# Kernel tuning notes

Hardware: AMD Instinct MI355X
Metric: run time of the kernel (lower is better)

The kernel has to match this reference:

```python
import jax, jax.numpy as jnp
import numpy as np

N_EMBD = 4096
N_HEAD = 2
HEAD_DIM = N_EMBD // N_HEAD  # 2048; note seq_len T must equal HEAD_DIM for the bias broadcast
B, T = 8, HEAD_DIM


def setup_inputs() -> dict:
    key = jax.random.key(0)
    ks = jax.random.split(key, 6)
    s = 1.0 / np.sqrt(N_EMBD)
    return {
        "x": jax.random.normal(ks[0], (B, T, N_EMBD), dtype=jnp.float32),
        "Wq": jax.random.normal(ks[1], (N_EMBD, N_EMBD), dtype=jnp.float32) * s,
        "Wk": jax.random.normal(ks[2], (N_EMBD, N_EMBD), dtype=jnp.float32) * s,
        "Wv": jax.random.normal(ks[3], (N_EMBD, N_EMBD), dtype=jnp.float32) * s,
        "Wo": jax.random.normal(ks[4], (N_EMBD, N_EMBD), dtype=jnp.float32) * s,
        "position_bias": jax.random.normal(ks[5], (N_HEAD, HEAD_DIM), dtype=jnp.float32) * 0.02,
    }


def reference(x, Wq, Wk, Wv, Wo, position_bias):
    Bb, Tt, C = x.shape
    H, D = N_HEAD, C // N_HEAD
    # nn.Linear(bias=False): y = x @ W.T
    q = (x @ Wq.T).reshape(Bb, Tt, H, D).transpose(0, 2, 1, 3)  # (B,H,T,D)
    k = (x @ Wk.T).reshape(Bb, Tt, H, D).transpose(0, 2, 1, 3)
    v = (x @ Wv.T).reshape(Bb, Tt, H, D).transpose(0, 2, 1, 3)
    scale = 1.0 / jnp.sqrt(jnp.asarray(D, dtype=x.dtype))
    scores = jnp.einsum("bhtd,bhsd->bhts", q, k) * scale  # (B,H,T,T)
    # position_bias (H,D) -> (1,H,1,D); broadcasts over key axis since D == T
    scores = scores + position_bias[None, :, None, :]
    atten = jax.nn.softmax(scores, axis=-1)  # mask=None, dropout=0.0 -> identity
    y = jnp.einsum("bhts,bhsd->bhtd", atten, v)  # (B,H,T,D)
    y = y.transpose(0, 2, 1, 3).reshape(Bb, Tt, C)
    y = y @ Wo.T
    return (y, atten)
```

## Files before the change

kernel.cpp:

```cpp
#include <hip/hip_runtime.h>
#include <hip/hip_bf16.h>
#include <cstdint>
#include <cstddef>


typedef short short8_t __attribute__((ext_vector_type(8)));
typedef float f32x4   __attribute__((ext_vector_type(4)));

__device__ __forceinline__ short f2bf(float f) {
  unsigned u = __builtin_bit_cast(unsigned, f);
  u = (u + 0x7FFFu + ((u >> 16) & 1u)) >> 16;
  return (short)u;
}

__device__ __forceinline__ short8_t cvt8(f32x4 a, f32x4 b) {
  short8_t r;
  r[0] = f2bf(a[0]); r[1] = f2bf(a[1]); r[2] = f2bf(a[2]); r[3] = f2bf(a[3]);
  r[4] = f2bf(b[0]); r[5] = f2bf(b[1]); r[6] = f2bf(b[2]); r[7] = f2bf(b[3]);
  return r;
}

__device__ __forceinline__ void gld_lds16(const void* g, void* l) {
  __builtin_amdgcn_global_load_lds(
      (const __attribute__((address_space(1))) void*)g,
      (__attribute__((address_space(3))) void*)l, 16, 0, 0);
}

__global__ __launch_bounds__(256)
void cvt_f32_bf16(const float* __restrict__ src, short* __restrict__ dst, int n8) {
  for (int i = blockIdx.x * blockDim.x + threadIdx.x; i < n8;
       i += gridDim.x * blockDim.x) {
    const f32x4* p = (const f32x4*)(src + (size_t)i * 8);
    f32x4 a = __builtin_nontemporal_load(p);
    f32x4 b = __builtin_nontemporal_load(p + 1);
    *(short8_t*)(dst + (size_t)i * 8) = cvt8(a, b);
  }
}

template<int MODE>
__global__ __launch_bounds__(512, 2)
void gemm256(const short* __restrict__ Ag, const short* __restrict__ Bg,
             void* __restrict__ Cg, const float* __restrict__ bias) {
  constexpr int K  = (MODE == 3 || MODE == 4) ? 2048 : 4096;
  constexpr int NS = K / 32;

  __shared__ short lds[65536];

  const int tid = threadIdx.x;

  const int bid = blockIdx.x;
  const int id  = (bid & 7) * (gridDim.x >> 3) + (bid >> 3);

  int m0, n0, z = 0;
  size_t aoff = 0, boff = 0;
  if constexpr (MODE == 3 || MODE == 4) {
    z  = id >> 6;
    m0 = ((id >> 3) & 7) << 8;
    n0 = (id & 7) << 8;
    aoff = boff = (size_t)z << 22;
  } else {
    m0 = (id >> 4) << 8;
    n0 = (id & 15) << 8;
  }

  const int r0 = tid >> 2;
  const int qs = ((tid & 3) ^ ((r0 >> 1) & 3)) << 3;
  const short* Ap0 = Ag + aoff + (size_t)(m0 + r0) * K + qs;
  const short* Ap1 = Ap0 + (size_t)128 * K;
  const short* Bp0 = Bg + boff + (size_t)(n0 + r0) * K + qs;
  const short* Bp1 = Bp0 + (size_t)128 * K;
  short* la0 = &lds[0]    + tid * 8;
  short* la1 = la0 + 4096;
  short* lb0 = &lds[8192] + tid * 8;
  short* lb1 = lb0 + 4096;

  auto STAGE = [&](int t) {
    const int s = (t & 3) * 16384;
    const int k = t * 32;
    gld_lds16(Ap0 + k, la0 + s);
    gld_lds16(Ap1 + k, la1 + s);
    gld_lds16(Bp0 + k, lb0 + s);
    gld_lds16(Bp1 + k, lb1 + s);
  };

  const int l  = tid & 63;
  const int fr = l & 15;
  const int kq = l >> 4;
  const int wm = (tid >> 8) << 7;
  const int wn = ((tid >> 6) & 3) << 6;
  const int slotP = (kq ^ ((fr >> 1) & 3)) << 3;
  const int aB = (wm + fr) * 32 + slotP;
  const int bB = 8192 + (wn + fr) * 32 + slotP;

  f32x4 acc[8][4] = {};
  short8_t fA[8], fB[4], gA[8], gB[4];

  auto phase = [&](int p, short8_t (&cA)[8], short8_t (&cB)[4],
                   short8_t (&nA)[8], short8_t (&nB)[4]) {
    if (p + 2 < NS) {
      asm volatile("s_waitcnt vmcnt(4)" ::: "memory");
    } else {
      asm volatile("s_waitcnt vmcnt(0)" ::: "memory");
    }
    __builtin_amdgcn_s_barrier();
    if (p + 3 < NS) STAGE(p + 3);
    if (p + 1 < NS) {
      const short* sl = &lds[((p + 1) & 3) * 16384];
#pragma unroll
      for (int m = 0; m < 8; ++m) nA[m] = *(const short8_t*)&sl[aB + m * 512];
#pragma unroll
      for (int n = 0; n < 4; ++n) nB[n] = *(const short8_t*)&sl[bB + n * 512];
    }
    __builtin_amdgcn_s_setprio(1);
#pragma unroll
    for (int m = 0; m < 8; ++m)
#pragma unroll
      for (int n = 0; n < 4; ++n)
        acc[m][n] = __builtin_amdgcn_mfma_f32_16x16x32_bf16(cA[m], cB[n], acc[m][n], 0, 0, 0);
    __builtin_amdgcn_s_setprio(0);
  };

  STAGE(0); STAGE(1); STAGE(2);
  asm volatile("s_waitcnt vmcnt(8)" ::: "memory");
  __builtin_amdgcn_s_barrier();
  {
    const short* sl = &lds[0];
#pragma unroll
    for (int m = 0; m < 8; ++m) fA[m] = *(const short8_t*)&sl[aB + m * 512];
#pragma unroll
    for (int n = 0; n < 4; ++n) fB[n] = *(const short8_t*)&sl[bB + n * 512];
  }

  for (int p = 0; p < NS; p += 2) {
    phase(p,     fA, fB, gA, gB);
    phase(p + 1, gA, gB, fA, fB);
  }

#pragma unroll
  for (int m = 0; m < 8; ++m) {
#pragma unroll
    for (int n = 0; n < 4; ++n) {
#pragma unroll
      for (int r = 0; r < 4; ++r) {
        const int gm = m0 + wm + m * 16 + kq * 4 + r;
        const int gn = n0 + wn + n * 16 + fr;
        const float v = acc[m][n][r];
        if constexpr (MODE == 0) {
          short* dst = (short*)Cg;
          const int bh = ((gm >> 11) << 1) + (gn >> 11);
          __builtin_nontemporal_store(f2bf(v),
            &dst[((size_t)bh << 22) + ((size_t)(gm & 2047) << 11) + (gn & 2047)]);
        } else if constexpr (MODE == 2) {
          short* dst = (short*)Cg;
          const int bh = ((gm >> 11) << 1) + (gn >> 11);
          __builtin_nontemporal_store(f2bf(v),
            &dst[((size_t)bh << 22) + ((size_t)(gn & 2047) << 11) + (gm & 2047)]);
        } else if constexpr (MODE == 3) {
          float* dst = (float*)Cg;
          const float sv = v * 0.022097086912079608f + bias[((z & 1) << 11) + gn];
          __builtin_nontemporal_store(sv,
            &dst[((size_t)z << 22) + ((size_t)gm << 11) + gn]);
        } else if constexpr (MODE == 4) {
          short* dst = (short*)Cg;
          const size_t row = ((size_t)(z >> 1) << 11) + gm;
          __builtin_nontemporal_store(f2bf(v),
            &dst[(row << 12) + ((size_t)(z & 1) << 11) + gn]);
        } else {
          float* dst = (float*)Cg;
          __builtin_nontemporal_store(v, &dst[(size_t)gm * 4096 + gn]);
        }
      }
    }
  }
}

__global__ __launch_bounds__(256)
void softmax_rows(float* __restrict__ attn, short* __restrict__ outb) {
  float* row  = attn + ((size_t)blockIdx.x << 11);
  short* rowb = outb + ((size_t)blockIdx.x << 11);
  const int tid = threadIdx.x;

  f32x4 v0 = __builtin_nontemporal_load((const f32x4*)(row + tid * 8));
  f32x4 v1 = __builtin_nontemporal_load((const f32x4*)(row + tid * 8 + 4));

  float m = fmaxf(fmaxf(fmaxf(v0[0], v0[1]), fmaxf(v0[2], v0[3])),
                  fmaxf(fmaxf(v1[0], v1[1]), fmaxf(v1[2], v1[3])));
#pragma unroll
  for (int off = 1; off < 64; off <<= 1) m = fmaxf(m, __shfl_xor(m, off));

  __shared__ float redm[4];
  __shared__ float reds[4];
  if ((tid & 63) == 0) redm[tid >> 6] = m;
  __syncthreads();
  m = fmaxf(fmaxf(redm[0], redm[1]), fmaxf(redm[2], redm[3]));

  float e[8];
#pragma unroll
  for (int i = 0; i < 4; ++i) e[i]     = expf(v0[i] - m);
#pragma unroll
  for (int i = 0; i < 4; ++i) e[4 + i] = expf(v1[i] - m);
  float s = 0.f;
#pragma unroll
  for (int i = 0; i < 8; ++i) s += e[i];
#pragma unroll
  for (int off = 1; off < 64; off <<= 1) s += __shfl_xor(s, off);
  if ((tid & 63) == 0) reds[tid >> 6] = s;
  __syncthreads();
  s = reds[0] + reds[1] + reds[2] + reds[3];

  const float inv = 1.0f / s;
  f32x4 o0, o1;
#pragma unroll
  for (int i = 0; i < 4; ++i) { o0[i] = e[i] * inv; o1[i] = e[4 + i] * inv; }
  __builtin_nontemporal_store(o0, (f32x4*)(row + tid * 8));
  __builtin_nontemporal_store(o1, (f32x4*)(row + tid * 8 + 4));
  *(short8_t*)(rowb + tid * 8) = cvt8(o0, o1);
}

extern "C" void kernel_launch(void* const* d_in, const int* in_sizes, int n_in,
                              void* d_out, int out_size, void* d_ws, size_t ws_size,
                              hipStream_t stream) {
  const float* x  = (const float*)d_in[0];
  const float* Wq = (const float*)d_in[1];
  const float* Wk = (const float*)d_in[2];
  const float* Wv = (const float*)d_in[3];
  const float* Wo = (const float*)d_in[4];
  const float* pb = (const float*)d_in[5];

  float* y_out = (float*)d_out;
  float* attn  = y_out + (size_t)8 * 2048 * 4096;

  const size_t NEED = 4ull * 67108864ull * 2ull;
  if (ws_size < NEED) return;
  short* buf0 = (short*)d_ws;
  short* buf1 = buf0 + 67108864;
  short* buf2 = buf1 + 67108864;
  short* buf3 = buf2 + 67108864;

  short* xb      = buf0;
  short* qb      = buf1;
  short* kb      = buf2;
  short* vtb     = buf3;
  short* wob     = buf0;
  short* attn_bf = buf1;
  short* yb      = buf2;
  short* wb      = (short*)attn;

  const dim3 blk512(512);
  const dim3 blk(256);
  const dim3 gcv(2048);
  const dim3 g1k(1024);

  cvt_f32_bf16<<<gcv, blk, 0, stream>>>(x, xb, 67108864 / 8);

  cvt_f32_bf16<<<gcv, blk, 0, stream>>>(Wq, wb, 16777216 / 8);
  gemm256<0><<<g1k, blk512, 0, stream>>>(xb, wb, qb, nullptr);
  cvt_f32_bf16<<<gcv, blk, 0, stream>>>(Wk, wb, 16777216 / 8);
  gemm256<0><<<g1k, blk512, 0, stream>>>(xb, wb, kb, nullptr);
  cvt_f32_bf16<<<gcv, blk, 0, stream>>>(Wv, wb, 16777216 / 8);
  gemm256<2><<<g1k, blk512, 0, stream>>>(xb, wb, vtb, nullptr);

  cvt_f32_bf16<<<gcv, blk, 0, stream>>>(Wo, wob, 16777216 / 8);

  gemm256<3><<<g1k, blk512, 0, stream>>>(qb, kb, attn, pb);
  softmax_rows<<<dim3(32768), blk, 0, stream>>>(attn, attn_bf);
  gemm256<4><<<g1k, blk512, 0, stream>>>(attn_bf, vtb, yb, nullptr);
  gemm256<5><<<g1k, blk512, 0, stream>>>(yb, wob, y_out, nullptr);
}
```

Before: 2.922 ms.

## Rework GEMM to 256 threads with 128x128 warp tiles and new LDS layout

Switches the 256x256-tile GEMM from 512 threads (8 waves, 128x64 per wave) to 256 threads (4 waves, 128x128 per wave, 64 accumulators per lane). It replaces the XOR-swizzled row-major LDS layout with a fragment-ordered layout where each lane reads a contiguous 16-byte chunk. It also drops the register double-buffered fragment prefetch in favour of a simpler single-stage load-then-MFMA loop. The goal is higher MFMA-to-LDS-read ratio per wave, at the cost of very high register pressure, one block per CU, and less latency hiding between LDS reads and MFMAs.

After: 3.347 ms. 1.15x slower.

```diff
diff --git a/kernel.cpp b/kernel.cpp
--- a/kernel.cpp
+++ b/kernel.cpp
@@ -38,7 +38,7 @@
 }
 
 template<int MODE>
-__global__ __launch_bounds__(512, 2)
+__global__ __launch_bounds__(256, 1)
 void gemm256(const short* __restrict__ Ag, const short* __restrict__ Bg,
              void* __restrict__ Cg, const float* __restrict__ bias) {
   constexpr int K  = (MODE == 3 || MODE == 4) ? 2048 : 4096;
@@ -63,83 +63,68 @@
     n0 = (id & 15) << 8;
   }
 
-  const int r0 = tid >> 2;
-  const int qs = ((tid & 3) ^ ((r0 >> 1) & 3)) << 3;
-  const short* Ap0 = Ag + aoff + (size_t)(m0 + r0) * K + qs;
-  const short* Ap1 = Ap0 + (size_t)128 * K;
-  const short* Bp0 = Bg + boff + (size_t)(n0 + r0) * K + qs;
-  const short* Bp1 = Bp0 + (size_t)128 * K;
-  short* la0 = &lds[0]    + tid * 8;
-  short* la1 = la0 + 4096;
-  short* lb0 = &lds[8192] + tid * 8;
-  short* lb1 = lb0 + 4096;
+  const int l = tid & 63;
+  const int w = tid >> 6;
+
+  const int srow = l & 15;
+  const int skol = (l >> 4) * 8;
+  const short* ApS = Ag + aoff + (size_t)(m0 + 64 * w + srow) * K + skol;
+  const short* BpS = Bg + boff + (size_t)(n0 + 64 * w + srow) * K + skol;
+  short* laS = &lds[(4 * w) * 512 + l * 8];
+  short* lbS = &lds[8192 + (4 * w) * 512 + l * 8];
 
   auto STAGE = [&](int t) {
-    const int s = (t & 3) * 16384;
-    const int k = t * 32;
-    gld_lds16(Ap0 + k, la0 + s);
-    gld_lds16(Ap1 + k, la1 + s);
-    gld_lds16(Bp0 + k, lb0 + s);
-    gld_lds16(Bp1 + k, lb1 + s);
+    const int s = (t & 3) << 14;
+    const size_t k = (size_t)t * 32;
+#pragma unroll
+    for (int j = 0; j < 4; ++j) {
+      gld_lds16(ApS + (size_t)j * 16 * K + k, laS + j * 512 + s);
+      gld_lds16(BpS + (size_t)j * 16 * K + k, lbS + j * 512 + s);
+    }
   };
 
-  const int l  = tid & 63;
+  const int aU = (w >> 1) * 8;
+  const int bU = (w & 1) * 8;
+  const int l8 = l * 8;
+
+  f32x4 acc[8][8] = {};
+
+  STAGE(0); STAGE(1); STAGE(2);
+
+  for (int p = 0; p < NS; ++p) {
+    if (p + 2 < NS)      asm volatile("s_waitcnt vmcnt(16)" ::: "memory");
+    else if (p + 1 < NS) asm volatile("s_waitcnt vmcnt(8)" ::: "memory");
+    else                 asm volatile("s_waitcnt vmcnt(0)" ::: "memory");
+    __builtin_amdgcn_s_barrier();
+
+    if (p + 3 < NS) STAGE(p + 3);
+
+    const int slot = (p & 3) << 14;
+    short8_t A[8], B[8];
+#pragma unroll
+    for (int i = 0; i < 8; ++i)
+      A[i] = *(const short8_t*)&lds[slot + (aU + i) * 512 + l8];
+#pragma unroll
+    for (int j = 0; j < 8; ++j)
+      B[j] = *(const short8_t*)&lds[slot + 8192 + (bU + j) * 512 + l8];
+
+    __builtin_amdgcn_s_setprio(1);
+#pragma unroll
+    for (int m = 0; m < 8; ++m)
+#pragma unroll
+      for (int n = 0; n < 8; ++n)
+        acc[m][n] = __builtin_amdgcn_mfma_f32_16x16x32_bf16(A[m], B[n], acc[m][n], 0, 0, 0);
+    __builtin_amdgcn_s_setprio(0);
+  }
+
   const int fr = l & 15;
   const int kq = l >> 4;
-  const int wm = (tid >> 8) << 7;
-  const int wn = ((tid >> 6) & 3) << 6;
-  const int slotP = (kq ^ ((fr >> 1) & 3)) << 3;
-  const int aB = (wm + fr) * 32 + slotP;
-  const int bB = 8192 + (wn + fr) * 32 + slotP;
-
-  f32x4 acc[8][4] = {};
-  short8_t fA[8], fB[4], gA[8], gB[4];
-
-  auto phase = [&](int p, short8_t (&cA)[8], short8_t (&cB)[4],
-                   short8_t (&nA)[8], short8_t (&nB)[4]) {
-    if (p + 2 < NS) {
-      asm volatile("s_waitcnt vmcnt(4)" ::: "memory");
-    } else {
-      asm volatile("s_waitcnt vmcnt(0)" ::: "memory");
-    }
-    __builtin_amdgcn_s_barrier();
-    if (p + 3 < NS) STAGE(p + 3);
-    if (p + 1 < NS) {
-      const short* sl = &lds[((p + 1) & 3) * 16384];
-#pragma unroll
-      for (int m = 0; m < 8; ++m) nA[m] = *(const short8_t*)&sl[aB + m * 512];
-#pragma unroll
-      for (int n = 0; n < 4; ++n) nB[n] = *(const short8_t*)&sl[bB + n * 512];
-    }
-    __builtin_amdgcn_s_setprio(1);
-#pragma unroll
-    for (int m = 0; m < 8; ++m)
-#pragma unroll
-      for (int n = 0; n < 4; ++n)
-        acc[m][n] = __builtin_amdgcn_mfma_f32_16x16x32_bf16(cA[m], cB[n], acc[m][n], 0, 0, 0);
-    __builtin_amdgcn_s_setprio(0);
-  };
-
-  STAGE(0); STAGE(1); STAGE(2);
-  asm volatile("s_waitcnt vmcnt(8)" ::: "memory");
-  __builtin_amdgcn_s_barrier();
-  {
-    const short* sl = &lds[0];
-#pragma unroll
-    for (int m = 0; m < 8; ++m) fA[m] = *(const short8_t*)&sl[aB + m * 512];
-#pragma unroll
-    for (int n = 0; n < 4; ++n) fB[n] = *(const short8_t*)&sl[bB + n * 512];
-  }
-
-  for (int p = 0; p < NS; p += 2) {
-    phase(p,     fA, fB, gA, gB);
-    phase(p + 1, gA, gB, fA, fB);
-  }
-
+  const int wm = (w >> 1) << 7;
+  const int wn = (w & 1) << 7;
 #pragma unroll
   for (int m = 0; m < 8; ++m) {
 #pragma unroll
-    for (int n = 0; n < 4; ++n) {
+    for (int n = 0; n < 8; ++n) {
 #pragma unroll
       for (int r = 0; r < 4; ++r) {
         const int gm = m0 + wm + m * 16 + kq * 4 + r;
@@ -246,7 +231,6 @@
   short* yb      = buf2;
   short* wb      = (short*)attn;
 
-  const dim3 blk512(512);
   const dim3 blk(256);
   const dim3 gcv(2048);
   const dim3 g1k(1024);
@@ -254,16 +238,16 @@
   cvt_f32_bf16<<<gcv, blk, 0, stream>>>(x, xb, 67108864 / 8);
 
   cvt_f32_bf16<<<gcv, blk, 0, stream>>>(Wq, wb, 16777216 / 8);
-  gemm256<0><<<g1k, blk512, 0, stream>>>(xb, wb, qb, nullptr);
+  gemm256<0><<<g1k, blk, 0, stream>>>(xb, wb, qb, nullptr);
   cvt_f32_bf16<<<gcv, blk, 0, stream>>>(Wk, wb, 16777216 / 8);
-  gemm256<0><<<g1k, blk512, 0, stream>>>(xb, wb, kb, nullptr);
+  gemm256<0><<<g1k, blk, 0, stream>>>(xb, wb, kb, nullptr);
   cvt_f32_bf16<<<gcv, blk, 0, stream>>>(Wv, wb, 16777216 / 8);
-  gemm256<2><<<g1k, blk512, 0, stream>>>(xb, wb, vtb, nullptr);
+  gemm256<2><<<g1k, blk, 0, stream>>>(xb, wb, vtb, nullptr);
 
   cvt_f32_bf16<<<gcv, blk, 0, stream>>>(Wo, wob, 16777216 / 8);
 
-  gemm256<3><<<g1k, blk512, 0, stream>>>(qb, kb, attn, pb);
+  gemm256<3><<<g1k, blk, 0, stream>>>(qb, kb, attn, pb);
   softmax_rows<<<dim3(32768), blk, 0, stream>>>(attn, attn_bf);
-  gemm256<4><<<g1k, blk512, 0, stream>>>(attn_bf, vtb, yb, nullptr);
-  gemm256<5><<<g1k, blk512, 0, stream>>>(yb, wob, y_out, nullptr);
-}
+  gemm256<4><<<g1k, blk, 0, stream>>>(attn_bf, vtb, yb, nullptr);
+  gemm256<5><<<g1k, blk, 0, stream>>>(yb, wob, y_out, nullptr);
+}
```

## Switch GEMM to 32x32x16 MFMA with fragment-native LDS layout

Applied to the files above, without the earlier changes.

Replaces the 16x16x32 bf16 MFMA tiling with 32x32x16 MFMAs, using 4x2 accumulator tiles of 16 floats per wave. The global-to-LDS staging is rearranged so each wave writes 32-row by 16-k fragments contiguously, and each lane reads its operand fragment with a linear 16-byte LDS load. This drops the XOR swizzle. The aim is fewer MFMA issues and fewer LDS reads per unit of work. The risk is LDS bank conflicts from the unswizzled layout and a more scattered epilogue store pattern.

After: 3.576 ms. +22.4%, slower.

```diff
diff --git a/kernel.cpp b/kernel.cpp
--- a/kernel.cpp
+++ b/kernel.cpp
@@ -6,6 +6,7 @@
 
 typedef short short8_t __attribute__((ext_vector_type(8)));
 typedef float f32x4   __attribute__((ext_vector_type(4)));
+typedef float f32x16  __attribute__((ext_vector_type(16)));
 
 __device__ __forceinline__ short f2bf(float f) {
   unsigned u = __builtin_bit_cast(unsigned, f);
@@ -63,88 +64,88 @@
     n0 = (id & 15) << 8;
   }
 
-  const int r0 = tid >> 2;
-  const int qs = ((tid & 3) ^ ((r0 >> 1) & 3)) << 3;
-  const short* Ap0 = Ag + aoff + (size_t)(m0 + r0) * K + qs;
-  const short* Ap1 = Ap0 + (size_t)128 * K;
-  const short* Bp0 = Bg + boff + (size_t)(n0 + r0) * K + qs;
-  const short* Bp1 = Bp0 + (size_t)128 * K;
-  short* la0 = &lds[0]    + tid * 8;
-  short* la1 = la0 + 4096;
-  short* lb0 = &lds[8192] + tid * 8;
-  short* lb1 = lb0 + 4096;
+  const int l = tid & 63;
+  const int w = tid >> 6;
+
+  const int srow = l & 31;
+  const int sk8  = (l >> 5) * 8;
+  const short* ApS = Ag + aoff + (size_t)(m0 + 32 * w + srow) * K + sk8;
+  const short* BpS = Bg + boff + (size_t)(n0 + 32 * w + srow) * K + sk8;
+  short* lA0 = &lds[(2 * w + 0) * 512 + l * 8];
+  short* lA1 = &lds[(2 * w + 1) * 512 + l * 8];
+  short* lB0 = &lds[8192 + (2 * w + 0) * 512 + l * 8];
+  short* lB1 = &lds[8192 + (2 * w + 1) * 512 + l * 8];
 
   auto STAGE = [&](int t) {
-    const int s = (t & 3) * 16384;
+    const int s = (t & 3) << 14;
     const int k = t * 32;
-    gld_lds16(Ap0 + k, la0 + s);
-    gld_lds16(Ap1 + k, la1 + s);
-    gld_lds16(Bp0 + k, lb0 + s);
-    gld_lds16(Bp1 + k, lb1 + s);
+    gld_lds16(ApS + k,      lA0 + s);
+    gld_lds16(ApS + k + 16, lA1 + s);
+    gld_lds16(BpS + k,      lB0 + s);
+    gld_lds16(BpS + k + 16, lB1 + s);
   };
 
-  const int l  = tid & 63;
-  const int fr = l & 15;
-  const int kq = l >> 4;
-  const int wm = (tid >> 8) << 7;
-  const int wn = ((tid >> 6) & 3) << 6;
-  const int slotP = (kq ^ ((fr >> 1) & 3)) << 3;
-  const int aB = (wm + fr) * 32 + slotP;
-  const int bB = 8192 + (wn + fr) * 32 + slotP;
-
-  f32x4 acc[8][4] = {};
-  short8_t fA[8], fB[4], gA[8], gB[4];
-
-  auto phase = [&](int p, short8_t (&cA)[8], short8_t (&cB)[4],
-                   short8_t (&nA)[8], short8_t (&nB)[4]) {
-    if (p + 2 < NS) {
-      asm volatile("s_waitcnt vmcnt(4)" ::: "memory");
-    } else {
-      asm volatile("s_waitcnt vmcnt(0)" ::: "memory");
-    }
+  const int g  = w >> 2;
+  const int h  = w & 3;
+  const int l8 = l * 8;
+
+  f32x16 acc[4][2] = {};
+  short8_t fA[4][2], fB[2][2], gA[4][2], gB[2][2];
+
+  auto LOADFRAG = [&](int p, short8_t (&A)[4][2], short8_t (&B)[2][2]) {
+    const int slot = (p & 3) << 14;
+#pragma unroll
+    for (int i = 0; i < 4; ++i)
+#pragma unroll
+      for (int kh = 0; kh < 2; ++kh)
+        A[i][kh] = *(const short8_t*)&lds[slot + ((g * 4 + i) * 2 + kh) * 512 + l8];
+#pragma unroll
+    for (int j = 0; j < 2; ++j)
+#pragma unroll
+      for (int kh = 0; kh < 2; ++kh)
+        B[j][kh] = *(const short8_t*)&lds[slot + 8192 + ((h * 2 + j) * 2 + kh) * 512 + l8];
+  };
+
+  auto phase = [&](int p, short8_t (&cA)[4][2], short8_t (&cB)[2][2],
+                   short8_t (&nA)[4][2], short8_t (&nB)[2][2]) {
+    if (p + 2 < NS) asm volatile("s_waitcnt vmcnt(4)" ::: "memory");
+    else            asm volatile("s_waitcnt vmcnt(0)" ::: "memory");
     __builtin_amdgcn_s_barrier();
     if (p + 3 < NS) STAGE(p + 3);
-    if (p + 1 < NS) {
-      const short* sl = &lds[((p + 1) & 3) * 16384];
-#pragma unroll
-      for (int m = 0; m < 8; ++m) nA[m] = *(const short8_t*)&sl[aB + m * 512];
-#pragma unroll
-      for (int n = 0; n < 4; ++n) nB[n] = *(const short8_t*)&sl[bB + n * 512];
-    }
+    if (p + 1 < NS) LOADFRAG(p + 1, nA, nB);
     __builtin_amdgcn_s_setprio(1);
 #pragma unroll
-    for (int m = 0; m < 8; ++m)
-#pragma unroll
-      for (int n = 0; n < 4; ++n)
-        acc[m][n] = __builtin_amdgcn_mfma_f32_16x16x32_bf16(cA[m], cB[n], acc[m][n], 0, 0, 0);
+    for (int i = 0; i < 4; ++i)
+#pragma unroll
+      for (int j = 0; j < 2; ++j)
+#pragma unroll
+        for (int kh = 0; kh < 2; ++kh)
+          acc[i][j] = __builtin_amdgcn_mfma_f32_32x32x16_bf16(cA[i][kh], cB[j][kh], acc[i][j], 0, 0, 0);
     __builtin_amdgcn_s_setprio(0);
   };
 
   STAGE(0); STAGE(1); STAGE(2);
   asm volatile("s_waitcnt vmcnt(8)" ::: "memory");
   __builtin_amdgcn_s_barrier();
-  {
-    const short* sl = &lds[0];
-#pragma unroll
-    for (int m = 0; m < 8; ++m) fA[m] = *(const short8_t*)&sl[aB + m * 512];
-#pragma unroll
-    for (int n = 0; n < 4; ++n) fB[n] = *(const short8_t*)&sl[bB + n * 512];
-  }
+  LOADFRAG(0, fA, fB);
 
   for (int p = 0; p < NS; p += 2) {
     phase(p,     fA, fB, gA, gB);
     phase(p + 1, gA, gB, fA, fB);
   }
 
-#pragma unroll
-  for (int m = 0; m < 8; ++m) {
-#pragma unroll
-    for (int n = 0; n < 4; ++n) {
-#pragma unroll
-      for (int r = 0; r < 4; ++r) {
-        const int gm = m0 + wm + m * 16 + kq * 4 + r;
-        const int gn = n0 + wn + n * 16 + fr;
-        const float v = acc[m][n][r];
+  const int col = l & 31;
+  const int rhi = (l >> 5) * 4;
+#pragma unroll
+  for (int i = 0; i < 4; ++i) {
+#pragma unroll
+    for (int j = 0; j < 2; ++j) {
+#pragma unroll
+      for (int r = 0; r < 16; ++r) {
+        const int row = (r & 3) + 8 * (r >> 2) + rhi;
+        const int gm  = m0 + g * 128 + i * 32 + row;
+        const int gn  = n0 + h * 64 + j * 32 + col;
+        const float v = acc[i][j][r];
         if constexpr (MODE == 0) {
           short* dst = (short*)Cg;
           const int bh = ((gm >> 11) << 1) + (gn >> 11);
@@ -162,9 +163,9 @@
             &dst[((size_t)z << 22) + ((size_t)gm << 11) + gn]);
         } else if constexpr (MODE == 4) {
           short* dst = (short*)Cg;
-          const size_t row = ((size_t)(z >> 1) << 11) + gm;
+          const size_t orow = ((size_t)(z >> 1) << 11) + gm;
           __builtin_nontemporal_store(f2bf(v),
-            &dst[(row << 12) + ((size_t)(z & 1) << 11) + gn]);
+            &dst[(orow << 12) + ((size_t)(z & 1) << 11) + gn]);
         } else {
           float* dst = (float*)Cg;
           __builtin_nontemporal_store(v, &dst[(size_t)gm * 4096 + gn]);
```
